# Performance work log

Measured on AMD Instinct MI355X. Metric: run time of the kernel, lower is better.

Reference implementation:

```python
import jax, jax.numpy as jnp
import numpy as np

B, HH, WW, C = 8, 128, 128, 128
NH = 4          # total heads; each branch uses NH//2
SS = 2          # split_size
EPS = 1e-5


def setup_inputs() -> dict:
    key = jax.random.key(0)
    ks = jax.random.split(key, 10)
    Ch = C // 2
    Dff = 4 * C
    return {
        "x": jax.random.normal(ks[0], (B, HH * WW, C), jnp.float32),
        "ln1_g": jnp.ones((C,), jnp.float32),
        "ln1_b": jnp.zeros((C,), jnp.float32),
        "w_qkv": jax.random.normal(ks[1], (3 * C, C), jnp.float32) * 0.02,
        "w_proj": jax.random.normal(ks[2], (C, C), jnp.float32) * 0.02,
        "b_proj": jnp.zeros((C,), jnp.float32),
        "conv_w0": jax.random.normal(ks[3], (Ch, 1, 3, 3), jnp.float32) * 0.02,
        "conv_b0": jnp.zeros((Ch,), jnp.float32),
        "conv_w1": jax.random.normal(ks[4], (Ch, 1, 3, 3), jnp.float32) * 0.02,
        "conv_b1": jnp.zeros((Ch,), jnp.float32),
        "ln2_g": jnp.ones((C,), jnp.float32),
        "ln2_b": jnp.zeros((C,), jnp.float32),
        "w1": jax.random.normal(ks[5], (Dff, C), jnp.float32) * 0.02,
        "b1": jnp.zeros((Dff,), jnp.float32),
        "w2": jax.random.normal(ks[6], (C, Dff), jnp.float32) * 0.02,
        "b2": jnp.zeros((C,), jnp.float32),
        "H": HH,
        "W": WW,
    }


def _layernorm(x, g, b):
    m = jnp.mean(x, axis=-1, keepdims=True)
    v = jnp.mean(jnp.square(x - m), axis=-1, keepdims=True)
    return (x - m) * jax.lax.rsqrt(v + EPS) * g + b


def _cswin_branch(q, k, v, conv_w, conv_b, H, W, H_sp, W_sp, heads):
    """q,k,v: [B, H*W, Ch] -> [B, H*W, Ch] cross-shaped-window LePE attention."""
    Bq, L, Ch = q.shape
    hd = Ch // heads
    T = H_sp * W_sp
    nh, nw = H // H_sp, W // W_sp

    def to_win(t):  # [B,L,Ch] -> [nW*B, heads, T, hd]
        t = t.reshape(Bq, nh, H_sp, nw, W_sp, Ch).transpose(0, 1, 3, 2, 4, 5)
        return t.reshape(-1, T, heads, hd).transpose(0, 2, 1, 3)

    qw, kw = to_win(q), to_win(k)

    # v as window images [nW*B, Ch, H_sp, W_sp] for depthwise LePE conv
    vimg = v.reshape(Bq, nh, H_sp, nw, W_sp, Ch).transpose(0, 1, 3, 5, 2, 4)
    vimg = vimg.reshape(-1, Ch, H_sp, W_sp)
    lepe = jax.lax.conv_general_dilated(
        vimg, conv_w, window_strides=(1, 1), padding="SAME",
        feature_group_count=Ch,
        dimension_numbers=("NCHW", "OIHW", "NCHW"),
    ) + conv_b[None, :, None, None]
    lepe = lepe.reshape(-1, heads, hd, T).transpose(0, 1, 3, 2)  # [nW*B,h,T,hd]
    vw = vimg.reshape(-1, heads, hd, T).transpose(0, 1, 3, 2)

    scale = hd ** -0.5
    attn = jnp.einsum("whtd,whsd->whts", qw * scale, kw)
    attn = jax.nn.softmax(attn, axis=-1)
    out = jnp.einsum("whts,whsd->whtd", attn, vw) + lepe  # [nW*B,h,T,hd]

    out = out.transpose(0, 2, 1, 3).reshape(-1, T, Ch)
    out = out.reshape(Bq, nh, nw, H_sp, W_sp, Ch).transpose(0, 1, 3, 2, 4, 5)
    return out.reshape(Bq, H * W, Ch)


def reference(x, ln1_g, ln1_b, w_qkv, w_proj, b_proj, conv_w0, conv_b0,
              conv_w1, conv_b1, ln2_g, ln2_b, w1, b1, w2, b2, H, W):
    Bx, L, Cx = x.shape
    Ch = Cx // 2
    heads = NH // 2

    img = _layernorm(x, ln1_g, ln1_b)
    qkv = (img @ w_qkv.T).reshape(Bx, L, 3, Cx)
    q, k, v = qkv[:, :, 0, :], qkv[:, :, 1, :], qkv[:, :, 2, :]

    # idx=0: horizontal stripes (H_sp=H, W_sp=SS); idx=1: vertical (H_sp=SS, W_sp=W)
    x1 = _cswin_branch(q[..., :Ch], k[..., :Ch], v[..., :Ch],
                       conv_w0, conv_b0, H, W, H, SS, heads)
    x2 = _cswin_branch(q[..., Ch:], k[..., Ch:], v[..., Ch:],
                       conv_w1, conv_b1, H, W, SS, W, heads)
    att = jnp.concatenate([x1, x2], axis=2)
    att = att @ w_proj.T + b_proj

    x = x + att
    h = _layernorm(x, ln2_g, ln2_b)
    h = jax.nn.gelu(h @ w1.T + b1, approximate=False) @ w2.T + b2
    return x + h
```

## Files before the change

kernel.cpp:

```cpp
#include <hip/hip_runtime.h>
#include <cstddef>


#define LDIM 16384
#define NTOK 131072
#define PLANE ((size_t)NTOK * 128)

typedef __attribute__((ext_vector_type(8))) short bf16x8;
typedef __attribute__((ext_vector_type(4))) float f32x4;

__device__ __forceinline__ unsigned short f2bf(float f) {
  union { float f; unsigned int i; } u; u.f = f;
  unsigned int r = u.i + 0x7fffu + ((u.i >> 16) & 1u);
  return (unsigned short)(r >> 16);
}
__device__ __forceinline__ float bflo(unsigned int u) {
  union { unsigned int i; float f; } x; x.i = u << 16; return x.f;
}
__device__ __forceinline__ float bfhi(unsigned int u) {
  union { unsigned int i; float f; } x; x.i = u & 0xffff0000u; return x.f;
}
__device__ __forceinline__ unsigned int pk(float a, float b) {
  return (unsigned)f2bf(a) | ((unsigned)f2bf(b) << 16);
}

__device__ __forceinline__ void async16(const unsigned short* g, unsigned short* l) {
  __builtin_amdgcn_global_load_lds(
      (const __attribute__((address_space(1))) unsigned int*)g,
      (__attribute__((address_space(3))) unsigned int*)l, 16, 0, 0);
}

__device__ __forceinline__ bf16x8 fragS(const unsigned short* base, int row, int c) {
  return *(const bf16x8*)(base + row * 128 + ((c ^ (row & 7)) << 3));
}

__device__ __forceinline__ void stageS128(const unsigned short* __restrict__ src, int rowStride,
                                          unsigned short* dst, int tid) {
  const int lane = tid & 63, wv = tid >> 6;
  #pragma unroll
  for (int i = 0; i < 8; i++) {
    const int base = i * 256 + wv * 64;
    const int f = base + lane;
    const int row = f >> 4, cs = f & 15, cg = cs ^ (row & 7);
    async16(src + (size_t)row * rowStride + (cg << 3), dst + (size_t)base * 8);
  }
}

__device__ __forceinline__ void stageS64(const unsigned short* __restrict__ src,
                                         unsigned short* dst, int tid) {
  const int lane = tid & 63, wv = tid >> 6;
  #pragma unroll
  for (int i = 0; i < 4; i++) {
    const int base = i * 256 + wv * 64;
    const int f = base + lane;
    const int row = f >> 4, cs = f & 15, cg = cs ^ (row & 7);
    async16(src + (size_t)row * 128 + (cg << 3), dst + (size_t)base * 8);
  }
}

__device__ __forceinline__ void gemmS(const unsigned short* As, const unsigned short* Bs,
                                      f32x4 acc[4][4], int wm, int wn, int q, int r) {
  #pragma unroll
  for (int kc = 0; kc < 4; kc++) {
    bf16x8 a[4], b[4];
    #pragma unroll
    for (int mt = 0; mt < 4; mt++) a[mt] = fragS(As, wm * 64 + mt * 16 + r, kc * 4 + q);
    #pragma unroll
    for (int nt = 0; nt < 4; nt++) b[nt] = fragS(Bs, wn * 64 + nt * 16 + r, kc * 4 + q);
    #pragma unroll
    for (int mt = 0; mt < 4; mt++)
      #pragma unroll
      for (int nt = 0; nt < 4; nt++)
        acc[mt][nt] = __builtin_amdgcn_mfma_f32_16x16x32_bf16(a[mt], b[nt], acc[mt][nt], 0, 0, 0);
  }
}

__device__ __forceinline__ void storeC(f32x4 acc[4][4], unsigned short* Cs,
                                       unsigned short* __restrict__ dst, int dstStride, int tid) {
  const int wv = tid >> 6, lane = tid & 63, q = lane >> 4, r = lane & 15;
  const int wm = wv & 1, wn = wv >> 1;
  #pragma unroll
  for (int mt = 0; mt < 4; mt++)
    #pragma unroll
    for (int nt = 0; nt < 4; nt++) {
      const int col = wn * 64 + nt * 16 + r;
      #pragma unroll
      for (int rg = 0; rg < 4; rg++) {
        const int row = wm * 64 + mt * 16 + q * 4 + rg;
        Cs[row * 128 + ((((col >> 3) ^ (row & 7)) << 3) | (col & 7))] = f2bf(acc[mt][nt][rg]);
      }
    }
  __syncthreads();
  #pragma unroll
  for (int i = 0; i < 8; i++) {
    const int f = tid + i * 256;
    const int row = f >> 4, cs = f & 15, cg = cs ^ (row & 7);
    *(uint4*)(dst + (size_t)row * dstStride + (cg << 3)) = *(const uint4*)(Cs + row * 128 + cs * 8);
  }
}

__device__ __forceinline__ float gelu_t(float x) {
  const float y = -2.3022083f * (x + 0.044715f * x * x * x);
  const float p = __builtin_amdgcn_exp2f(y);
  return x * __builtin_amdgcn_rcpf(1.f + p);
}

__global__ void k_prep(const float* __restrict__ wq, const float* __restrict__ wp,
                       const float* __restrict__ w1, const float* __restrict__ w2,
                       unsigned short* __restrict__ wb)
{
  const int id = blockIdx.x * 256 + threadIdx.x;
  const float* src; int off;
  if (id < 12288)      { src = wq; off = id; }
  else if (id < 16384) { src = wp; off = id - 12288; }
  else if (id < 32768) { src = w1; off = id - 16384; }
  else                 { src = w2; off = id - 32768; }
  const float4 v = *(const float4*)(src + (size_t)off * 4);
  uint2 u; u.x = pk(v.x, v.y); u.y = pk(v.z, v.w);
  *(uint2*)(wb + (size_t)id * 4) = u;
}

__global__ __launch_bounds__(256, 2) void k_ln_qkv(
    const float* __restrict__ x, const float* __restrict__ g, const float* __restrict__ bb,
    const unsigned short* __restrict__ wqkvb, unsigned short* __restrict__ qkv)
{
  __shared__ unsigned short xs[128 * 128];
  __shared__ unsigned short ws[128 * 128];
  __shared__ float redS[128][2], redQ[128][2];
  const int tid = threadIdx.x;
  const long m0 = (long)blockIdx.x * 128;
  {
    const int m = tid >> 1, hf = tid & 1;
    const float4* xg = (const float4*)(x + (size_t)(m0 + m) * 128 + hf * 64);
    float4 xv[16];
    #pragma unroll
    for (int i = 0; i < 16; i++) xv[i] = xg[i];
    float s1 = 0.f, s2 = 0.f;
    #pragma unroll
    for (int i = 0; i < 16; i++) {
      s1 += xv[i].x + xv[i].y + xv[i].z + xv[i].w;
      s2 += xv[i].x * xv[i].x + xv[i].y * xv[i].y + xv[i].z * xv[i].z + xv[i].w * xv[i].w;
    }
    redS[m][hf] = s1; redQ[m][hf] = s2;
    __syncthreads();
    const float mean = (redS[m][0] + redS[m][1]) * (1.f / 128.f);
    const float var  = (redQ[m][0] + redQ[m][1]) * (1.f / 128.f) - mean * mean;
    const float rs = rsqrtf(var + 1e-5f);
    const float4* g4 = (const float4*)(g + hf * 64);
    const float4* b4 = (const float4*)(bb + hf * 64);
    #pragma unroll
    for (int i = 0; i < 8; i++) {
      float4 v0 = xv[2 * i], v1 = xv[2 * i + 1];
      float4 g0 = g4[2 * i], g1 = g4[2 * i + 1], p0 = b4[2 * i], p1 = b4[2 * i + 1];
      uint4 u;
      u.x = pk((v0.x - mean) * rs * g0.x + p0.x, (v0.y - mean) * rs * g0.y + p0.y);
      u.y = pk((v0.z - mean) * rs * g0.z + p0.z, (v0.w - mean) * rs * g0.w + p0.w);
      u.z = pk((v1.x - mean) * rs * g1.x + p1.x, (v1.y - mean) * rs * g1.y + p1.y);
      u.w = pk((v1.z - mean) * rs * g1.z + p1.z, (v1.w - mean) * rs * g1.w + p1.w);
      const int c = hf * 8 + i;
      *(uint4*)&xs[m * 128 + ((c ^ (m & 7)) << 3)] = u;
    }
  }
  const int lane = tid & 63, q = lane >> 4, r = lane & 15;
  const int wv = tid >> 6, wm = wv & 1, wn = wv >> 1;
  for (int nc = 0; nc < 3; nc++) {
    __syncthreads();
    stageS128(wqkvb + (size_t)nc * 16384, 128, ws, tid);
    __syncthreads();
    f32x4 acc[4][4];
    #pragma unroll
    for (int a = 0; a < 4; a++)
      #pragma unroll
      for (int b = 0; b < 4; b++) acc[a][b] = f32x4{0.f, 0.f, 0.f, 0.f};
    gemmS(xs, ws, acc, wm, wn, q, r);
    __syncthreads();
    storeC(acc, ws, qkv + (size_t)nc * PLANE + (size_t)m0 * 128, 128, tid);
  }
}

__global__ __launch_bounds__(256, 2) void k_attn(
    const unsigned short* __restrict__ qkv,
    const float* __restrict__ conv_w0, const float* __restrict__ conv_b0,
    const float* __restrict__ conv_w1, const float* __restrict__ conv_b1,
    unsigned short* __restrict__ att)
{
  __shared__ unsigned short Kt[256][40];
  __shared__ unsigned short Vt[32][264];
  __shared__ unsigned short Ps[4][64][72];
  const unsigned short* kpl = qkv + PLANE;
  const unsigned short* vpl = qkv + 2 * PLANE;
  const int t = threadIdx.x;
  const int win = blockIdx.x, head = blockIdx.y, br = blockIdx.z;
  const int bimg = win >> 6, widx = win & 63;
  const int c0 = br * 64 + head * 32;
  const int lgWs = (br == 0) ? 1 : 7;
  const int Wsm1 = (1 << lgWs) - 1;
  const long base = (long)bimg * LDIM + ((br == 0) ? widx * 2 : widx * 256);

  {
    const long tj = base + (long)(t >> lgWs) * 128 + (t & Wsm1);
    const uint4* kp = (const uint4*)(kpl + (size_t)tj * 128 + c0);
    uint4 k0v = kp[0], k1v = kp[1], k2v = kp[2], k3v = kp[3];
    *(uint4*)&Kt[t][0]  = k0v;  *(uint4*)&Kt[t][8]  = k1v;
    *(uint4*)&Kt[t][16] = k2v;  *(uint4*)&Kt[t][24] = k3v;
    const uint4* vp = (const uint4*)(vpl + (size_t)tj * 128 + c0);
    uint4 vv[4] = {vp[0], vp[1], vp[2], vp[3]};
    const unsigned short* vs = (const unsigned short*)vv;
    #pragma unroll
    for (int d = 0; d < 32; d++) Vt[d][t] = vs[d];
  }
  const int wave = t >> 6, lane = t & 63, q = lane >> 4, r = lane & 15;
  const int qbase = wave * 64;
  bf16x8 qf[4];
  #pragma unroll
  for (int mt = 0; mt < 4; mt++) {
    const int row = qbase + mt * 16 + r;
    const long tok = base + (long)(row >> lgWs) * 128 + (row & Wsm1);
    qf[mt] = *(const bf16x8*)(qkv + (size_t)tok * 128 + c0 + q * 8);
  }
  __syncthreads();

  const float factor = 0.17677669529663687f * 1.44269504088896341f;
  f32x4 Oacc[4][2];
  float psum[4][4];
  #pragma unroll
  for (int mt = 0; mt < 4; mt++) {
    Oacc[mt][0] = f32x4{0.f, 0.f, 0.f, 0.f};
    Oacc[mt][1] = f32x4{0.f, 0.f, 0.f, 0.f};
    #pragma unroll
    for (int rg = 0; rg < 4; rg++) psum[mt][rg] = 0.f;
  }

  for (int kc = 0; kc < 4; kc++) {
    bf16x8 kb[4];
    #pragma unroll
    for (int nt = 0; nt < 4; nt++) kb[nt] = *(const bf16x8*)&Kt[kc * 64 + nt * 16 + r][q * 8];
    f32x4 s[4][4];
    #pragma unroll
    for (int mt = 0; mt < 4; mt++)
      #pragma unroll
      for (int nt = 0; nt < 4; nt++) {
        f32x4 z = f32x4{0.f, 0.f, 0.f, 0.f};
        s[mt][nt] = __builtin_amdgcn_mfma_f32_16x16x32_bf16(qf[mt], kb[nt], z, 0, 0, 0);
      }
    #pragma unroll
    for (int mt = 0; mt < 4; mt++)
      #pragma unroll
      for (int nt = 0; nt < 4; nt++)
        #pragma unroll
        for (int rg = 0; rg < 4; rg++) {
          const float p = __builtin_amdgcn_exp2f(s[mt][nt][rg] * factor);
          psum[mt][rg] += p;
          Ps[wave][mt * 16 + q * 4 + rg][nt * 16 + r] = f2bf(p);
        }
    #pragma unroll
    for (int kst = 0; kst < 2; kst++) {
      bf16x8 pa[4], vb[2];
      #pragma unroll
      for (int mt = 0; mt < 4; mt++) pa[mt] = *(const bf16x8*)&Ps[wave][mt * 16 + r][kst * 32 + q * 8];
      #pragma unroll
      for (int nto = 0; nto < 2; nto++) vb[nto] = *(const bf16x8*)&Vt[nto * 16 + r][kc * 64 + kst * 32 + q * 8];
      #pragma unroll
      for (int mt = 0; mt < 4; mt++)
        #pragma unroll
        for (int nto = 0; nto < 2; nto++)
          Oacc[mt][nto] = __builtin_amdgcn_mfma_f32_16x16x32_bf16(pa[mt], vb[nto], Oacc[mt][nto], 0, 0, 0);
    }
  }

  #pragma unroll
  for (int mt = 0; mt < 4; mt++)
    #pragma unroll
    for (int rg = 0; rg < 4; rg++) {
      float v = psum[mt][rg];
      v += __shfl_xor(v, 1); v += __shfl_xor(v, 2);
      v += __shfl_xor(v, 4); v += __shfl_xor(v, 8);
      psum[mt][rg] = __builtin_amdgcn_rcpf(v);
    }

  const float* cw = br ? conv_w1 : conv_w0;
  const float* cb = br ? conv_b1 : conv_b0;
  float wle[2][9], ble[2];
  #pragma unroll
  for (int nto = 0; nto < 2; nto++) {
    const int ch = head * 32 + nto * 16 + r;
    ble[nto] = cb[ch];
    #pragma unroll
    for (int tp = 0; tp < 9; tp++) wle[nto][tp] = cw[ch * 9 + tp];
  }
  const int WsW = 1 << lgWs;
  const int HsW = 256 >> lgWs;

  #pragma unroll
  for (int mt = 0; mt < 4; mt++)
    #pragma unroll
    for (int rg = 0; rg < 4; rg++) {
      const int row = qbase + mt * 16 + q * 4 + rg;
      const int ii = row >> lgWs, jj = row & Wsm1;
      const long tok = base + (long)ii * 128 + jj;
      float lep0 = ble[0], lep1 = ble[1];
      #pragma unroll
      for (int di = -1; di <= 1; di++) {
        if ((unsigned)(ii + di) >= (unsigned)HsW) continue;
        #pragma unroll
        for (int dj = -1; dj <= 1; dj++) {
          if ((unsigned)(jj + dj) >= (unsigned)WsW) continue;
          const int nb = row + di * WsW + dj;
          const int tap = (di + 1) * 3 + (dj + 1);
          lep0 = fmaf(bflo(Vt[r][nb]),      wle[0][tap], lep0);
          lep1 = fmaf(bflo(Vt[16 + r][nb]), wle[1][tap], lep1);
        }
      }
      const float pr = psum[mt][rg];
      att[(size_t)tok * 128 + c0 + r]      = f2bf(Oacc[mt][0][rg] * pr + lep0);
      att[(size_t)tok * 128 + c0 + 16 + r] = f2bf(Oacc[mt][1][rg] * pr + lep1);
    }
}

__global__ __launch_bounds__(256, 2) void k_projmlp(
    const unsigned short* __restrict__ att, const unsigned short* __restrict__ wprojb,
    const float* __restrict__ b_proj, const float* __restrict__ x,
    const float* __restrict__ g, const float* __restrict__ bb,
    const unsigned short* __restrict__ w1b, const unsigned short* __restrict__ w2b,
    const float* __restrict__ b1, const float* __restrict__ b2,
    float* __restrict__ out)
{
  __shared__ unsigned short hs[64 * 128];
  __shared__ unsigned short ws[128 * 128];
  __shared__ unsigned short xs[64 * 128];
  __shared__ float redS[64][4], redQ[64][4];
  const int tid = threadIdx.x;
  const long m0 = (long)blockIdx.x * 64;
  const int lane = tid & 63, q = lane >> 4, r = lane & 15, wv = tid >> 6;

  stageS64(att + (size_t)m0 * 128, hs, tid);
  stageS128(wprojb, 128, ws, tid);

  float xv[4][2][4];
  #pragma unroll
  for (int mt = 0; mt < 4; mt++)
    #pragma unroll
    for (int nt = 0; nt < 2; nt++) {
      const int col = wv * 32 + nt * 16 + r;
      #pragma unroll
      for (int rg = 0; rg < 4; rg++)
        xv[mt][nt][rg] = x[(size_t)(m0 + mt * 16 + q * 4 + rg) * 128 + col];
    }
  float bpv[2], gv[2], bv2[2];
  #pragma unroll
  for (int nt = 0; nt < 2; nt++) {
    const int col = wv * 32 + nt * 16 + r;
    bpv[nt] = b_proj[col]; gv[nt] = g[col]; bv2[nt] = bb[col];
  }
  __syncthreads();

  f32x4 xres[4][2];
  #pragma unroll
  for (int mt = 0; mt < 4; mt++) { xres[mt][0] = f32x4{0.f,0.f,0.f,0.f}; xres[mt][1] = f32x4{0.f,0.f,0.f,0.f}; }
  #pragma unroll
  for (int kc = 0; kc < 4; kc++) {
    bf16x8 a[4], b[2];
    #pragma unroll
    for (int mt = 0; mt < 4; mt++) a[mt] = fragS(hs, mt * 16 + r, kc * 4 + q);
    #pragma unroll
    for (int nt = 0; nt < 2; nt++) b[nt] = fragS(ws, wv * 32 + nt * 16 + r, kc * 4 + q);
    #pragma unroll
    for (int mt = 0; mt < 4; mt++)
      #pragma unroll
      for (int nt = 0; nt < 2; nt++)
        xres[mt][nt] = __builtin_amdgcn_mfma_f32_16x16x32_bf16(a[mt], b[nt], xres[mt][nt], 0, 0, 0);
  }
  #pragma unroll
  for (int mt = 0; mt < 4; mt++)
    #pragma unroll
    for (int nt = 0; nt < 2; nt++)
      #pragma unroll
      for (int rg = 0; rg < 4; rg++)
        xres[mt][nt][rg] += xv[mt][nt][rg] + bpv[nt];

  #pragma unroll
  for (int mt = 0; mt < 4; mt++)
    #pragma unroll
    for (int rg = 0; rg < 4; rg++) {
      float s1 = xres[mt][0][rg] + xres[mt][1][rg];
      float s2 = xres[mt][0][rg] * xres[mt][0][rg] + xres[mt][1][rg] * xres[mt][1][rg];
      s1 += __shfl_xor(s1, 1); s1 += __shfl_xor(s1, 2); s1 += __shfl_xor(s1, 4); s1 += __shfl_xor(s1, 8);
      s2 += __shfl_xor(s2, 1); s2 += __shfl_xor(s2, 2); s2 += __shfl_xor(s2, 4); s2 += __shfl_xor(s2, 8);
      if (r == 0) { const int row = mt * 16 + q * 4 + rg; redS[row][wv] = s1; redQ[row][wv] = s2; }
    }
  __syncthreads();
  #pragma unroll
  for (int mt = 0; mt < 4; mt++)
    #pragma unroll
    for (int rg = 0; rg < 4; rg++) {
      const int row = mt * 16 + q * 4 + rg;
      const float s1 = redS[row][0] + redS[row][1] + redS[row][2] + redS[row][3];
      const float s2 = redQ[row][0] + redQ[row][1] + redQ[row][2] + redQ[row][3];
      const float mean = s1 * (1.f / 128.f);
      const float var  = s2 * (1.f / 128.f) - mean * mean;
      const float rs = rsqrtf(var + 1e-5f);
      #pragma unroll
      for (int nt = 0; nt < 2; nt++) {
        const int col = wv * 32 + nt * 16 + r;
        const float v = (xres[mt][nt][rg] - mean) * rs * gv[nt] + bv2[nt];
        xs[row * 128 + ((((col >> 3) ^ (row & 7)) << 3) | (col & 7))] = f2bf(v);
      }
    }

  f32x4 oacc[4][2];
  #pragma unroll
  for (int mt = 0; mt < 4; mt++) { oacc[mt][0] = f32x4{0.f,0.f,0.f,0.f}; oacc[mt][1] = f32x4{0.f,0.f,0.f,0.f}; }

  for (int nc = 0; nc < 4; nc++) {
    __syncthreads();
    stageS128(w1b + (size_t)nc * 16384, 128, ws, tid);
    __syncthreads();
    f32x4 h[4][2];
    #pragma unroll
    for (int mt = 0; mt < 4; mt++) { h[mt][0] = f32x4{0.f,0.f,0.f,0.f}; h[mt][1] = f32x4{0.f,0.f,0.f,0.f}; }
    #pragma unroll
    for (int kc = 0; kc < 4; kc++) {
      bf16x8 a[4], b[2];
      #pragma unroll
      for (int mt = 0; mt < 4; mt++) a[mt] = fragS(xs, mt * 16 + r, kc * 4 + q);
      #pragma unroll
      for (int nt = 0; nt < 2; nt++) b[nt] = fragS(ws, wv * 32 + nt * 16 + r, kc * 4 + q);
      #pragma unroll
      for (int mt = 0; mt < 4; mt++)
        #pragma unroll
        for (int nt = 0; nt < 2; nt++)
          h[mt][nt] = __builtin_amdgcn_mfma_f32_16x16x32_bf16(a[mt], b[nt], h[mt][nt], 0, 0, 0);
    }
    __syncthreads();
    #pragma unroll
    for (int mt = 0; mt < 4; mt++)
      #pragma unroll
      for (int nt = 0; nt < 2; nt++) {
        const int col = wv * 32 + nt * 16 + r;
        const float bv = b1[nc * 128 + col];
        #pragma unroll
        for (int rg = 0; rg < 4; rg++) {
          const int rw = mt * 16 + q * 4 + rg;
          hs[rw * 128 + ((((col >> 3) ^ (rw & 7)) << 3) | (col & 7))] = f2bf(gelu_t(h[mt][nt][rg] + bv));
        }
      }
    stageS128(w2b + (size_t)nc * 128, 512, ws, tid);
    __syncthreads();
    #pragma unroll
    for (int kc = 0; kc < 4; kc++) {
      bf16x8 a[4], b[2];
      #pragma unroll
      for (int mt = 0; mt < 4; mt++) a[mt] = fragS(hs, mt * 16 + r, kc * 4 + q);
      #pragma unroll
      for (int nt = 0; nt < 2; nt++) b[nt] = fragS(ws, wv * 32 + nt * 16 + r, kc * 4 + q);
      #pragma unroll
      for (int mt = 0; mt < 4; mt++)
        #pragma unroll
        for (int nt = 0; nt < 2; nt++)
          oacc[mt][nt] = __builtin_amdgcn_mfma_f32_16x16x32_bf16(a[mt], b[nt], oacc[mt][nt], 0, 0, 0);
    }
  }
  #pragma unroll
  for (int mt = 0; mt < 4; mt++)
    #pragma unroll
    for (int nt = 0; nt < 2; nt++) {
      const int col = wv * 32 + nt * 16 + r;
      const float bv = b2[col];
      #pragma unroll
      for (int rg = 0; rg < 4; rg++) {
        const size_t idx = (size_t)(m0 + mt * 16 + q * 4 + rg) * 128 + col;
        out[idx] = xres[mt][nt][rg] + bv + oacc[mt][nt][rg];
      }
    }
}

extern "C" void kernel_launch(void* const* d_in, const int* in_sizes, int n_in,
                              void* d_out, int out_size, void* d_ws, size_t ws_size,
                              hipStream_t stream) {
  const float* x       = (const float*)d_in[0];
  const float* ln1_g   = (const float*)d_in[1];
  const float* ln1_b   = (const float*)d_in[2];
  const float* w_qkv   = (const float*)d_in[3];
  const float* w_proj  = (const float*)d_in[4];
  const float* b_proj  = (const float*)d_in[5];
  const float* conv_w0 = (const float*)d_in[6];
  const float* conv_b0 = (const float*)d_in[7];
  const float* conv_w1 = (const float*)d_in[8];
  const float* conv_b1 = (const float*)d_in[9];
  const float* ln2_g   = (const float*)d_in[10];
  const float* ln2_b   = (const float*)d_in[11];
  const float* w1      = (const float*)d_in[12];
  const float* b1      = (const float*)d_in[13];
  const float* w2      = (const float*)d_in[14];
  const float* b2      = (const float*)d_in[15];
  float* out = (float*)d_out;

  unsigned short* qkv = (unsigned short*)d_ws;
  unsigned short* att = qkv;
  unsigned short* wb  = qkv + 3 * PLANE;
  unsigned short* wqkvb  = wb;
  unsigned short* wprojb = wb + 49152;
  unsigned short* w1b    = wb + 65536;
  unsigned short* w2b    = wb + 131072;

  k_prep<<<dim3(192), 256, 0, stream>>>(w_qkv, w_proj, w1, w2, wb);
  k_ln_qkv<<<dim3(NTOK / 128), 256, 0, stream>>>(x, ln1_g, ln1_b, wqkvb, qkv);
  k_attn<<<dim3(512, 2, 2), 256, 0, stream>>>(qkv, conv_w0, conv_b0, conv_w1, conv_b1, att);
  k_projmlp<<<dim3(NTOK / 64), 256, 0, stream>>>(att, wprojb, b_proj, x, ln2_g, ln2_b,
                                                 w1b, w2b, b1, b2, out);
}
```

Measured before the change: 359.5 us.

## Load GEMM weight fragments directly from global instead of staging through LDS

```diff
diff --git a/kernel.cpp b/kernel.cpp
--- a/kernel.cpp
+++ b/kernel.cpp
@@ -34,16 +34,8 @@
   return *(const bf16x8*)(base + row * 128 + ((c ^ (row & 7)) << 3));
 }
 
-__device__ __forceinline__ void stageS128(const unsigned short* __restrict__ src, int rowStride,
-                                          unsigned short* dst, int tid) {
-  const int lane = tid & 63, wv = tid >> 6;
-  #pragma unroll
-  for (int i = 0; i < 8; i++) {
-    const int base = i * 256 + wv * 64;
-    const int f = base + lane;
-    const int row = f >> 4, cs = f & 15, cg = cs ^ (row & 7);
-    async16(src + (size_t)row * rowStride + (cg << 3), dst + (size_t)base * 8);
-  }
+__device__ __forceinline__ bf16x8 ldw(const unsigned short* p) {
+  return *(const bf16x8*)p;
 }
 
 __device__ __forceinline__ void stageS64(const unsigned short* __restrict__ src,
@@ -55,23 +47,6 @@
     const int f = base + lane;
     const int row = f >> 4, cs = f & 15, cg = cs ^ (row & 7);
     async16(src + (size_t)row * 128 + (cg << 3), dst + (size_t)base * 8);
-  }
-}
-
-__device__ __forceinline__ void gemmS(const unsigned short* As, const unsigned short* Bs,
-                                      f32x4 acc[4][4], int wm, int wn, int q, int r) {
-  #pragma unroll
-  for (int kc = 0; kc < 4; kc++) {
-    bf16x8 a[4], b[4];
-    #pragma unroll
-    for (int mt = 0; mt < 4; mt++) a[mt] = fragS(As, wm * 64 + mt * 16 + r, kc * 4 + q);
-    #pragma unroll
-    for (int nt = 0; nt < 4; nt++) b[nt] = fragS(Bs, wn * 64 + nt * 16 + r, kc * 4 + q);
-    #pragma unroll
-    for (int mt = 0; mt < 4; mt++)
-      #pragma unroll
-      for (int nt = 0; nt < 4; nt++)
-        acc[mt][nt] = __builtin_amdgcn_mfma_f32_16x16x32_bf16(a[mt], b[nt], acc[mt][nt], 0, 0, 0);
   }
 }
 
@@ -125,7 +100,7 @@
     const unsigned short* __restrict__ wqkvb, unsigned short* __restrict__ qkv)
 {
   __shared__ unsigned short xs[128 * 128];
-  __shared__ unsigned short ws[128 * 128];
+  __shared__ unsigned short Cs[128 * 128];
   __shared__ float redS[128][2], redQ[128][2];
   const int tid = threadIdx.x;
   const long m0 = (long)blockIdx.x * 128;
@@ -163,18 +138,29 @@
   }
   const int lane = tid & 63, q = lane >> 4, r = lane & 15;
   const int wv = tid >> 6, wm = wv & 1, wn = wv >> 1;
+  __syncthreads();
   for (int nc = 0; nc < 3; nc++) {
-    __syncthreads();
-    stageS128(wqkvb + (size_t)nc * 16384, 128, ws, tid);
-    __syncthreads();
     f32x4 acc[4][4];
     #pragma unroll
     for (int a = 0; a < 4; a++)
       #pragma unroll
       for (int b = 0; b < 4; b++) acc[a][b] = f32x4{0.f, 0.f, 0.f, 0.f};
-    gemmS(xs, ws, acc, wm, wn, q, r);
-    __syncthreads();
-    storeC(acc, ws, qkv + (size_t)nc * PLANE + (size_t)m0 * 128, 128, tid);
+    const unsigned short* wbase = wqkvb + (size_t)(nc * 128 + wn * 64) * 128;
+    #pragma unroll
+    for (int kc = 0; kc < 4; kc++) {
+      bf16x8 a[4], b[4];
+      #pragma unroll
+      for (int mt = 0; mt < 4; mt++) a[mt] = fragS(xs, wm * 64 + mt * 16 + r, kc * 4 + q);
+      #pragma unroll
+      for (int nt = 0; nt < 4; nt++) b[nt] = ldw(wbase + (nt * 16 + r) * 128 + kc * 32 + q * 8);
+      #pragma unroll
+      for (int mt = 0; mt < 4; mt++)
+        #pragma unroll
+        for (int nt = 0; nt < 4; nt++)
+          acc[mt][nt] = __builtin_amdgcn_mfma_f32_16x16x32_bf16(a[mt], b[nt], acc[mt][nt], 0, 0, 0);
+    }
+    if (nc) __syncthreads();
+    storeC(acc, Cs, qkv + (size_t)nc * PLANE + (size_t)m0 * 128, 128, tid);
   }
 }
 
@@ -317,7 +303,7 @@
     }
 }
 
-__global__ __launch_bounds__(256, 2) void k_projmlp(
+__global__ __launch_bounds__(256, 3) void k_projmlp(
     const unsigned short* __restrict__ att, const unsigned short* __restrict__ wprojb,
     const float* __restrict__ b_proj, const float* __restrict__ x,
     const float* __restrict__ g, const float* __restrict__ bb,
@@ -326,7 +312,6 @@
     float* __restrict__ out)
 {
   __shared__ unsigned short hs[64 * 128];
-  __shared__ unsigned short ws[128 * 128];
   __shared__ unsigned short xs[64 * 128];
   __shared__ float redS[64][4], redQ[64][4];
   const int tid = threadIdx.x;
@@ -334,7 +319,6 @@
   const int lane = tid & 63, q = lane >> 4, r = lane & 15, wv = tid >> 6;
 
   stageS64(att + (size_t)m0 * 128, hs, tid);
-  stageS128(wprojb, 128, ws, tid);
 
   float xv[4][2][4];
   #pragma unroll
@@ -357,18 +341,21 @@
   f32x4 xres[4][2];
   #pragma unroll
   for (int mt = 0; mt < 4; mt++) { xres[mt][0] = f32x4{0.f,0.f,0.f,0.f}; xres[mt][1] = f32x4{0.f,0.f,0.f,0.f}; }
-  #pragma unroll
-  for (int kc = 0; kc < 4; kc++) {
-    bf16x8 a[4], b[2];
-    #pragma unroll
-    for (int mt = 0; mt < 4; mt++) a[mt] = fragS(hs, mt * 16 + r, kc * 4 + q);
-    #pragma unroll
-    for (int nt = 0; nt < 2; nt++) b[nt] = fragS(ws, wv * 32 + nt * 16 + r, kc * 4 + q);
-    #pragma unroll
-    for (int mt = 0; mt < 4; mt++)
-      #pragma unroll
-      for (int nt = 0; nt < 2; nt++)
-        xres[mt][nt] = __builtin_amdgcn_mfma_f32_16x16x32_bf16(a[mt], b[nt], xres[mt][nt], 0, 0, 0);
+  {
+    const unsigned short* wpbase = wprojb + (size_t)(wv * 32) * 128;
+    #pragma unroll
+    for (int kc = 0; kc < 4; kc++) {
+      bf16x8 a[4], b[2];
+      #pragma unroll
+      for (int mt = 0; mt < 4; mt++) a[mt] = fragS(hs, mt * 16 + r, kc * 4 + q);
+      #pragma unroll
+      for (int nt = 0; nt < 2; nt++) b[nt] = ldw(wpbase + (nt * 16 + r) * 128 + kc * 32 + q * 8);
+      #pragma unroll
+      for (int mt = 0; mt < 4; mt++)
+        #pragma unroll
+        for (int nt = 0; nt < 2; nt++)
+          xres[mt][nt] = __builtin_amdgcn_mfma_f32_16x16x32_bf16(a[mt], b[nt], xres[mt][nt], 0, 0, 0);
+    }
   }
   #pragma unroll
   for (int mt = 0; mt < 4; mt++)
@@ -413,25 +400,25 @@
 
   for (int nc = 0; nc < 4; nc++) {
     __syncthreads();
-    stageS128(w1b + (size_t)nc * 16384, 128, ws, tid);
-    __syncthreads();
     f32x4 h[4][2];
     #pragma unroll
     for (int mt = 0; mt < 4; mt++) { h[mt][0] = f32x4{0.f,0.f,0.f,0.f}; h[mt][1] = f32x4{0.f,0.f,0.f,0.f}; }
-    #pragma unroll
-    for (int kc = 0; kc < 4; kc++) {
-      bf16x8 a[4], b[2];
-      #pragma unroll
-      for (int mt = 0; mt < 4; mt++) a[mt] = fragS(xs, mt * 16 + r, kc * 4 + q);
-      #pragma unroll
-      for (int nt = 0; nt < 2; nt++) b[nt] = fragS(ws, wv * 32 + nt * 16 + r, kc * 4 + q);
-      #pragma unroll
-      for (int mt = 0; mt < 4; mt++)
-        #pragma unroll
-        for (int nt = 0; nt < 2; nt++)
-          h[mt][nt] = __builtin_amdgcn_mfma_f32_16x16x32_bf16(a[mt], b[nt], h[mt][nt], 0, 0, 0);
-    }
-    __syncthreads();
+    {
+      const unsigned short* w1base = w1b + (size_t)(nc * 128 + wv * 32) * 128;
+      #pragma unroll
+      for (int kc = 0; kc < 4; kc++) {
+        bf16x8 a[4], b[2];
+        #pragma unroll
+        for (int mt = 0; mt < 4; mt++) a[mt] = fragS(xs, mt * 16 + r, kc * 4 + q);
+        #pragma unroll
+        for (int nt = 0; nt < 2; nt++) b[nt] = ldw(w1base + (nt * 16 + r) * 128 + kc * 32 + q * 8);
+        #pragma unroll
+        for (int mt = 0; mt < 4; mt++)
+          #pragma unroll
+          for (int nt = 0; nt < 2; nt++)
+            h[mt][nt] = __builtin_amdgcn_mfma_f32_16x16x32_bf16(a[mt], b[nt], h[mt][nt], 0, 0, 0);
+      }
+    }
     #pragma unroll
     for (int mt = 0; mt < 4; mt++)
       #pragma unroll
@@ -444,20 +431,22 @@
           hs[rw * 128 + ((((col >> 3) ^ (rw & 7)) << 3) | (col & 7))] = f2bf(gelu_t(h[mt][nt][rg] + bv));
         }
       }
-    stageS128(w2b + (size_t)nc * 128, 512, ws, tid);
     __syncthreads();
-    #pragma unroll
-    for (int kc = 0; kc < 4; kc++) {
-      bf16x8 a[4], b[2];
-      #pragma unroll
-      for (int mt = 0; mt < 4; mt++) a[mt] = fragS(hs, mt * 16 + r, kc * 4 + q);
-      #pragma unroll
-      for (int nt = 0; nt < 2; nt++) b[nt] = fragS(ws, wv * 32 + nt * 16 + r, kc * 4 + q);
-      #pragma unroll
-      for (int mt = 0; mt < 4; mt++)
-        #pragma unroll
-        for (int nt = 0; nt < 2; nt++)
-          oacc[mt][nt] = __builtin_amdgcn_mfma_f32_16x16x32_bf16(a[mt], b[nt], oacc[mt][nt], 0, 0, 0);
+    {
+      const unsigned short* w2base = w2b + (size_t)(wv * 32) * 512 + nc * 128;
+      #pragma unroll
+      for (int kc = 0; kc < 4; kc++) {
+        bf16x8 a[4], b[2];
+        #pragma unroll
+        for (int mt = 0; mt < 4; mt++) a[mt] = fragS(hs, mt * 16 + r, kc * 4 + q);
+        #pragma unroll
+        for (int nt = 0; nt < 2; nt++) b[nt] = ldw(w2base + (nt * 16 + r) * 512 + kc * 32 + q * 8);
+        #pragma unroll
+        for (int mt = 0; mt < 4; mt++)
+          #pragma unroll
+          for (int nt = 0; nt < 2; nt++)
+            oacc[mt][nt] = __builtin_amdgcn_mfma_f32_16x16x32_bf16(a[mt], b[nt], oacc[mt][nt], 0, 0, 0);
+      }
     }
   }
   #pragma unroll
```

Result: slower. 378.3 us (+5.2%).

## Give each wave a private weight slice and prefetch next MLP weights in projmlp

Applied to the files above, without the earlier changes.

```diff
diff --git a/kernel.cpp b/kernel.cpp
--- a/kernel.cpp
+++ b/kernel.cpp
@@ -28,6 +28,20 @@
   __builtin_amdgcn_global_load_lds(
       (const __attribute__((address_space(1))) unsigned int*)g,
       (__attribute__((address_space(3))) unsigned int*)l, 16, 0, 0);
+}
+
+__device__ __forceinline__ void wait_lgkm0() {
+  asm volatile("s_waitcnt lgkmcnt(0)" ::: "memory");
+  __builtin_amdgcn_sched_barrier(0);
+}
+__device__ __forceinline__ void wait_vm0() {
+  asm volatile("s_waitcnt vmcnt(0)" ::: "memory");
+  __builtin_amdgcn_sched_barrier(0);
+}
+__device__ __forceinline__ void barrier_lgkm() {
+  asm volatile("s_waitcnt lgkmcnt(0)" ::: "memory");
+  __builtin_amdgcn_s_barrier();
+  __builtin_amdgcn_sched_barrier(0);
 }
 
 __device__ __forceinline__ bf16x8 fragS(const unsigned short* base, int row, int c) {
@@ -55,6 +69,16 @@
     const int f = base + lane;
     const int row = f >> 4, cs = f & 15, cg = cs ^ (row & 7);
     async16(src + (size_t)row * 128 + (cg << 3), dst + (size_t)base * 8);
+  }
+}
+
+__device__ __forceinline__ void stageW32(const unsigned short* __restrict__ src, int rowStride,
+                                         unsigned short* dstRegion, int lane) {
+  #pragma unroll
+  for (int i = 0; i < 8; i++) {
+    const int rowLocal = i * 4 + (lane >> 4);
+    const int cs = lane & 15, cg = cs ^ (rowLocal & 7);
+    async16(src + (size_t)rowLocal * rowStride + (cg << 3), dstRegion + i * 512);
   }
 }
 
@@ -326,15 +350,16 @@
     float* __restrict__ out)
 {
   __shared__ unsigned short hs[64 * 128];
+  __shared__ unsigned short xs[64 * 128];
   __shared__ unsigned short ws[128 * 128];
-  __shared__ unsigned short xs[64 * 128];
   __shared__ float redS[64][4], redQ[64][4];
   const int tid = threadIdx.x;
   const long m0 = (long)blockIdx.x * 64;
   const int lane = tid & 63, q = lane >> 4, r = lane & 15, wv = tid >> 6;
+  unsigned short* wsW = ws + (size_t)wv * 32 * 128;
 
   stageS64(att + (size_t)m0 * 128, hs, tid);
-  stageS128(wprojb, 128, ws, tid);
+  stageW32(wprojb + (size_t)(wv * 32) * 128, 128, wsW, lane);
 
   float xv[4][2][4];
   #pragma unroll
@@ -346,11 +371,13 @@
       for (int rg = 0; rg < 4; rg++)
         xv[mt][nt][rg] = x[(size_t)(m0 + mt * 16 + q * 4 + rg) * 128 + col];
     }
-  float bpv[2], gv[2], bv2[2];
+  float bpv[2], gv[2], bv2[2], b1v[4][2], b2v[2];
   #pragma unroll
   for (int nt = 0; nt < 2; nt++) {
     const int col = wv * 32 + nt * 16 + r;
-    bpv[nt] = b_proj[col]; gv[nt] = g[col]; bv2[nt] = bb[col];
+    bpv[nt] = b_proj[col]; gv[nt] = g[col]; bv2[nt] = bb[col]; b2v[nt] = b2[col];
+    #pragma unroll
+    for (int nc = 0; nc < 4; nc++) b1v[nc][nt] = b1[nc * 128 + col];
   }
   __syncthreads();
 
@@ -370,6 +397,9 @@
       for (int nt = 0; nt < 2; nt++)
         xres[mt][nt] = __builtin_amdgcn_mfma_f32_16x16x32_bf16(a[mt], b[nt], xres[mt][nt], 0, 0, 0);
   }
+  wait_lgkm0();
+  stageW32(w1b + (size_t)(wv * 32) * 128, 128, wsW, lane);
+
   #pragma unroll
   for (int mt = 0; mt < 4; mt++)
     #pragma unroll
@@ -388,7 +418,7 @@
       s2 += __shfl_xor(s2, 1); s2 += __shfl_xor(s2, 2); s2 += __shfl_xor(s2, 4); s2 += __shfl_xor(s2, 8);
       if (r == 0) { const int row = mt * 16 + q * 4 + rg; redS[row][wv] = s1; redQ[row][wv] = s2; }
     }
-  __syncthreads();
+  barrier_lgkm();
   #pragma unroll
   for (int mt = 0; mt < 4; mt++)
     #pragma unroll
@@ -406,66 +436,78 @@
         xs[row * 128 + ((((col >> 3) ^ (row & 7)) << 3) | (col & 7))] = f2bf(v);
       }
     }
+  barrier_lgkm();
 
   f32x4 oacc[4][2];
   #pragma unroll
   for (int mt = 0; mt < 4; mt++) { oacc[mt][0] = f32x4{0.f,0.f,0.f,0.f}; oacc[mt][1] = f32x4{0.f,0.f,0.f,0.f}; }
 
   for (int nc = 0; nc < 4; nc++) {
-    __syncthreads();
-    stageS128(w1b + (size_t)nc * 16384, 128, ws, tid);
-    __syncthreads();
+    wait_vm0();
+    bf16x8 b1f[4][2];
+    #pragma unroll
+    for (int kc = 0; kc < 4; kc++)
+      #pragma unroll
+      for (int nt = 0; nt < 2; nt++)
+        b1f[kc][nt] = fragS(ws, wv * 32 + nt * 16 + r, kc * 4 + q);
+    wait_lgkm0();
+    stageW32(w2b + (size_t)(wv * 32) * 512 + nc * 128, 512, wsW, lane);
     f32x4 h[4][2];
     #pragma unroll
     for (int mt = 0; mt < 4; mt++) { h[mt][0] = f32x4{0.f,0.f,0.f,0.f}; h[mt][1] = f32x4{0.f,0.f,0.f,0.f}; }
     #pragma unroll
     for (int kc = 0; kc < 4; kc++) {
-      bf16x8 a[4], b[2];
+      bf16x8 a[4];
       #pragma unroll
       for (int mt = 0; mt < 4; mt++) a[mt] = fragS(xs, mt * 16 + r, kc * 4 + q);
-      #pragma unroll
-      for (int nt = 0; nt < 2; nt++) b[nt] = fragS(ws, wv * 32 + nt * 16 + r, kc * 4 + q);
       #pragma unroll
       for (int mt = 0; mt < 4; mt++)
         #pragma unroll
         for (int nt = 0; nt < 2; nt++)
-          h[mt][nt] = __builtin_amdgcn_mfma_f32_16x16x32_bf16(a[mt], b[nt], h[mt][nt], 0, 0, 0);
-    }
-    __syncthreads();
+          h[mt][nt] = __builtin_amdgcn_mfma_f32_16x16x32_bf16(a[mt], b1f[kc][nt], h[mt][nt], 0, 0, 0);
+    }
+    barrier_lgkm();
     #pragma unroll
     for (int mt = 0; mt < 4; mt++)
       #pragma unroll
       for (int nt = 0; nt < 2; nt++) {
         const int col = wv * 32 + nt * 16 + r;
-        const float bv = b1[nc * 128 + col];
+        const float bv = b1v[nc][nt];
         #pragma unroll
         for (int rg = 0; rg < 4; rg++) {
           const int rw = mt * 16 + q * 4 + rg;
           hs[rw * 128 + ((((col >> 3) ^ (rw & 7)) << 3) | (col & 7))] = f2bf(gelu_t(h[mt][nt][rg] + bv));
         }
       }
-    stageS128(w2b + (size_t)nc * 128, 512, ws, tid);
-    __syncthreads();
+    barrier_lgkm();
+    wait_vm0();
+    bf16x8 b2f[4][2];
+    #pragma unroll
+    for (int kc = 0; kc < 4; kc++)
+      #pragma unroll
+      for (int nt = 0; nt < 2; nt++)
+        b2f[kc][nt] = fragS(ws, wv * 32 + nt * 16 + r, kc * 4 + q);
+    wait_lgkm0();
+    if (nc < 3)
+      stageW32(w1b + (size_t)((nc + 1) * 128 + wv * 32) * 128, 128, wsW, lane);
     #pragma unroll
     for (int kc = 0; kc < 4; kc++) {
-      bf16x8 a[4], b[2];
+      bf16x8 a[4];
       #pragma unroll
       for (int mt = 0; mt < 4; mt++) a[mt] = fragS(hs, mt * 16 + r, kc * 4 + q);
-      #pragma unroll
-      for (int nt = 0; nt < 2; nt++) b[nt] = fragS(ws, wv * 32 + nt * 16 + r, kc * 4 + q);
       #pragma unroll
       for (int mt = 0; mt < 4; mt++)
         #pragma unroll
         for (int nt = 0; nt < 2; nt++)
-          oacc[mt][nt] = __builtin_amdgcn_mfma_f32_16x16x32_bf16(a[mt], b[nt], oacc[mt][nt], 0, 0, 0);
+          oacc[mt][nt] = __builtin_amdgcn_mfma_f32_16x16x32_bf16(a[mt], b2f[kc][nt], oacc[mt][nt], 0, 0, 0);
     }
   }
   #pragma unroll
   for (int mt = 0; mt < 4; mt++)
     #pragma unroll
     for (int nt = 0; nt < 2; nt++) {
+      const float bv = b2v[nt];
       const int col = wv * 32 + nt * 16 + r;
-      const float bv = b2[col];
       #pragma unroll
       for (int rg = 0; rg < 4; rg++) {
         const size_t idx = (size_t)(m0 + mt * 16 + q * 4 + rg) * 128 + col;
```

Result: faster. 345.2 us (-4.0%).
